# Kernel optimization log

Measured on AMD Instinct MI355X. Metric: run time of the kernel, lower is better.

## Reference

```python
import jax, jax.numpy as jnp
import numpy as np

EPS = 1e-9


def setup_inputs() -> dict:
    key = jax.random.key(0)
    k1, k2, k3, k4 = jax.random.split(key, 4)
    B, D, U = 1024, 512, 512
    x = jax.random.normal(k1, (B, D), dtype=jnp.float32)
    w = jax.random.normal(k2, (D, U), dtype=jnp.float32)
    p = jax.random.normal(k3, (D, U), dtype=jnp.float32)
    b = jax.random.normal(k4, (U,), dtype=jnp.float32)
    return {"x": x, "w": w, "p": p, "b": b}


def reference(x, w, p, b):
    # x: [B, D]; w, p: [D, U]; b: [U]
    xe = x[..., None] + EPS                      # [B, D, 1]
    abs_pow = jnp.abs(xe) ** p                   # [B, D, U]
    is_neg = xe < 0                              # [B, D, 1]
    odd_mask = jnp.mod(p, 2) != 0                # [D, U]
    signed = jnp.where(odd_mask & is_neg, -abs_pow, abs_pow)
    z = jnp.sum(w * signed, axis=1) + b          # [B, U]
    return z  # linear activation
```

## Files before the change

kernel.cpp:

```cpp
#include <hip/hip_runtime.h>
#include <math.h>

#define EPS 1e-9f

constexpr int Bn = 1024, Dn = 512, Un = 512;
constexpr int BM = 32;
constexpr int BU = 64;
constexpr int DK = 16;
constexpr int SPLITD = 8;
constexpr int DPB = Dn / SPLITD;
constexpr int NCHUNK = DPB / DK;

typedef float v4f __attribute__((ext_vector_type(4)));

__device__ __forceinline__ int swz(int d) { return ((d >> 2) & 3) << 3; }

template <bool USE_WS>
__global__ __launch_bounds__(256, 4) void power_layer(
    const float* __restrict__ x, const float* __restrict__ w,
    const float* __restrict__ p, const float* __restrict__ bias,
    float* __restrict__ outp)
{
    __shared__ float sL[DK][BM];
    __shared__ float sP[DK][BU];
    __shared__ float sW[DK][BU];
    __shared__ float sWX[DK][BU];

    const int tid = threadIdx.x;
    const int tx  = tid & 15;
    const int ty  = tid >> 4;
    const int tx4 = tx * 4;
    const int ty2 = ty * 2;
    const int ub = blockIdx.x * BU;
    const int bb = blockIdx.y * BM;
    const int d0 = blockIdx.z * DPB;

    const int xr  = tid >> 2;
    const int xdq = (tid & 3) << 2;
    const int pd  = tid >> 4;
    const int puq = (tid & 15) << 2;

    float4 xv = {}, pv = {}, wv = {};
    if (tid < 128)
        xv = *reinterpret_cast<const float4*>(&x[(size_t)(bb + xr) * Dn + d0 + xdq]);
    {
        const size_t gi = (size_t)(d0 + pd) * Un + ub + puq;
        pv = *reinterpret_cast<const float4*>(&p[gi]);
        wv = *reinterpret_cast<const float4*>(&w[gi]);
    }

    v4f acc[2] = {};

    for (int ch = 0; ch < NCHUNK; ++ch) {
        float Lenc[4];
        if (tid < 128) {
            const float* xs = reinterpret_cast<const float*>(&xv);
            #pragma unroll
            for (int j = 0; j < 4; ++j) {
                const float xe = xs[j] + EPS;
                const float La = __builtin_amdgcn_logf(fabsf(xe)) + 64.0f;
                Lenc[j] = (xe < 0.0f) ? -La : La;
            }
        }
        float4 wxv;
        {
            const float* ps  = reinterpret_cast<const float*>(&pv);
            const float* wsv = reinterpret_cast<const float*>(&wv);
            float* wxs = reinterpret_cast<float*>(&wxv);
            #pragma unroll
            for (int j = 0; j < 4; ++j) {
                const bool odd = (fmodf(ps[j], 2.0f) != 0.0f);
                wxs[j] = odd ? -wsv[j] : wsv[j];
            }
        }

        __syncthreads();
        if (tid < 128) {
            #pragma unroll
            for (int j = 0; j < 4; ++j) {
                const int dd = xdq + j;
                sL[dd][xr ^ swz(dd)] = Lenc[j];
            }
        }
        *reinterpret_cast<float4*>(&sP[pd][puq])  = pv;
        *reinterpret_cast<float4*>(&sW[pd][puq])  = wv;
        *reinterpret_cast<float4*>(&sWX[pd][puq]) = wxv;
        __syncthreads();

        if (ch + 1 < NCHUNK) {
            const int db = d0 + (ch + 1) * DK;
            if (tid < 128)
                xv = *reinterpret_cast<const float4*>(&x[(size_t)(bb + xr) * Dn + db + xdq]);
            const size_t gi = (size_t)(db + pd) * Un + ub + puq;
            pv = *reinterpret_cast<const float4*>(&p[gi]);
            wv = *reinterpret_cast<const float4*>(&w[gi]);
        }

        #pragma unroll 4
        for (int d = 0; d < DK; ++d) {
            const float2 Lv = *reinterpret_cast<const float2*>(&sL[d][ty2 ^ swz(d)]);
            const v4f    Pv = *reinterpret_cast<const v4f*>(&sP[d][tx4]);
            const float* Ls = reinterpret_cast<const float*>(&Lv);

            #pragma unroll
            for (int r = 0; r < 2; ++r) {
                const float Ld = fabsf(Ls[r]) - 64.0f;
                const bool  ng = Ls[r] < 0.0f;
                const v4f Wsel = *reinterpret_cast<const v4f*>(
                    ng ? &sWX[d][tx4] : &sW[d][tx4]);

                const v4f t = Pv * Ld;
                v4f e;
                #pragma unroll
                for (int c = 0; c < 4; ++c)
                    e[c] = __builtin_amdgcn_exp2f(t[c]);
                acc[r] = __builtin_elementwise_fma(Wsel, e, acc[r]);
            }
        }
        __syncthreads();
    }

    if (USE_WS) {
        float* dst = outp + ((size_t)blockIdx.z * Bn + bb + ty2) * Un + ub + tx4;
        #pragma unroll
        for (int r = 0; r < 2; ++r)
            *reinterpret_cast<v4f*>(dst + (size_t)r * Un) = acc[r];
    } else {
        if (blockIdx.z == 0) {
            const v4f bv = *reinterpret_cast<const v4f*>(&bias[ub + tx4]);
            #pragma unroll
            for (int r = 0; r < 2; ++r)
                acc[r] += bv;
        }
        #pragma unroll
        for (int r = 0; r < 2; ++r) {
            const int row = bb + ty2 + r;
            #pragma unroll
            for (int c = 0; c < 4; ++c)
                atomicAdd(&outp[(size_t)row * Un + ub + tx4 + c], acc[r][c]);
        }
    }
}

__global__ __launch_bounds__(256) void reduce_ws(
    const float* __restrict__ ws, const float* __restrict__ bias,
    float* __restrict__ out)
{
    const int nf4 = (Bn * Un) / 4;
    const int i = blockIdx.x * 256 + threadIdx.x;
    if (i >= nf4) return;
    const v4f* w4 = reinterpret_cast<const v4f*>(ws);
    v4f a = w4[i];
    #pragma unroll
    for (int z = 1; z < SPLITD; ++z)
        a += w4[(size_t)z * nf4 + i];
    a += reinterpret_cast<const v4f*>(bias)[i & (Un / 4 - 1)];
    reinterpret_cast<v4f*>(out)[i] = a;
}

extern "C" void kernel_launch(void* const* d_in, const int* in_sizes, int n_in,
                              void* d_out, int out_size, void* d_ws, size_t ws_size,
                              hipStream_t stream) {
    const float* x = (const float*)d_in[0];
    const float* w = (const float*)d_in[1];
    const float* p = (const float*)d_in[2];
    const float* b = (const float*)d_in[3];
    float* out = (float*)d_out;

    const dim3 grid(Un / BU, Bn / BM, SPLITD);
    const size_t need = (size_t)SPLITD * Bn * Un * sizeof(float);

    if (ws_size >= need) {
        float* wsf = (float*)d_ws;
        power_layer<true><<<grid, dim3(256), 0, stream>>>(x, w, p, b, wsf);
        reduce_ws<<<dim3((Bn * Un / 4 + 255) / 256), dim3(256), 0, stream>>>(wsf, b, out);
    } else {
        hipMemsetAsync(out, 0, (size_t)out_size * sizeof(float), stream);
        power_layer<false><<<grid, dim3(256), 0, stream>>>(x, w, p, b, out);
    }
}
```

Measured before the change: 109.5 us.

## Double-buffer P/W tiles and precompute full log(x) slab once per block

Precomputes the log-encoded x values for the block's whole D slice into shared memory up front, using all 256 threads, so x is no longer reloaded and re-logged per chunk. The P, W and sign-flipped W tiles are double-buffered, which cuts the per-chunk barriers from three to one. Shared memory grows, which may reduce occupancy, and the swizzle changes to suit the larger L array.

```diff
diff --git a/kernel.cpp b/kernel.cpp
--- a/kernel.cpp
+++ b/kernel.cpp
@@ -13,7 +13,7 @@
 
 typedef float v4f __attribute__((ext_vector_type(4)));
 
-__device__ __forceinline__ int swz(int d) { return ((d >> 2) & 3) << 3; }
+__device__ __forceinline__ int swzL(int d) { return ((d >> 3) & 7) << 2; }
 
 template <bool USE_WS>
 __global__ __launch_bounds__(256, 4) void power_layer(
@@ -21,10 +21,10 @@
     const float* __restrict__ p, const float* __restrict__ bias,
     float* __restrict__ outp)
 {
-    __shared__ float sL[DK][BM];
-    __shared__ float sP[DK][BU];
-    __shared__ float sW[DK][BU];
-    __shared__ float sWX[DK][BU];
+    __shared__ float sL[DPB][BM];
+    __shared__ float sP [2][DK][BU];
+    __shared__ float sW [2][DK][BU];
+    __shared__ float sWX[2][DK][BU];
 
     const int tid = threadIdx.x;
     const int tx  = tid & 15;
@@ -35,71 +35,67 @@
     const int bb = blockIdx.y * BM;
     const int d0 = blockIdx.z * DPB;
 
-    const int xr  = tid >> 2;
-    const int xdq = (tid & 3) << 2;
     const int pd  = tid >> 4;
     const int puq = (tid & 15) << 2;
 
-    float4 xv = {}, pv = {}, wv = {};
-    if (tid < 128)
-        xv = *reinterpret_cast<const float4*>(&x[(size_t)(bb + xr) * Dn + d0 + xdq]);
+    {
+        const int xr = tid >> 3;
+        const int xd = (tid & 7) << 3;
+        const int sw = (tid & 7) << 2;
+        const float* xrow = &x[(size_t)(bb + xr) * Dn + d0 + xd];
+        const float4 xa = *reinterpret_cast<const float4*>(xrow);
+        const float4 xb = *reinterpret_cast<const float4*>(xrow + 4);
+        const float* s0 = reinterpret_cast<const float*>(&xa);
+        const float* s1 = reinterpret_cast<const float*>(&xb);
+        #pragma unroll
+        for (int j = 0; j < 4; ++j) {
+            const float xe = s0[j] + EPS;
+            const float La = __builtin_amdgcn_logf(fabsf(xe)) + 64.0f;
+            sL[xd + j][xr ^ sw] = (xe < 0.0f) ? -La : La;
+        }
+        #pragma unroll
+        for (int j = 0; j < 4; ++j) {
+            const float xe = s1[j] + EPS;
+            const float La = __builtin_amdgcn_logf(fabsf(xe)) + 64.0f;
+            sL[xd + 4 + j][xr ^ sw] = (xe < 0.0f) ? -La : La;
+        }
+    }
     {
         const size_t gi = (size_t)(d0 + pd) * Un + ub + puq;
-        pv = *reinterpret_cast<const float4*>(&p[gi]);
-        wv = *reinterpret_cast<const float4*>(&w[gi]);
+        const float4 pv = *reinterpret_cast<const float4*>(&p[gi]);
+        const float4 wv = *reinterpret_cast<const float4*>(&w[gi]);
+        const float* ps  = reinterpret_cast<const float*>(&pv);
+        const float* wsv = reinterpret_cast<const float*>(&wv);
+        float4 wxv;
+        float* wxs = reinterpret_cast<float*>(&wxv);
+        #pragma unroll
+        for (int j = 0; j < 4; ++j) {
+            const bool odd = (fmodf(ps[j], 2.0f) != 0.0f);
+            wxs[j] = odd ? -wsv[j] : wsv[j];
+        }
+        *reinterpret_cast<float4*>(&sP [0][pd][puq]) = pv;
+        *reinterpret_cast<float4*>(&sW [0][pd][puq]) = wv;
+        *reinterpret_cast<float4*>(&sWX[0][pd][puq]) = wxv;
     }
+    __syncthreads();
 
     v4f acc[2] = {};
 
     for (int ch = 0; ch < NCHUNK; ++ch) {
-        float Lenc[4];
-        if (tid < 128) {
-            const float* xs = reinterpret_cast<const float*>(&xv);
-            #pragma unroll
-            for (int j = 0; j < 4; ++j) {
-                const float xe = xs[j] + EPS;
-                const float La = __builtin_amdgcn_logf(fabsf(xe)) + 64.0f;
-                Lenc[j] = (xe < 0.0f) ? -La : La;
-            }
-        }
-        float4 wxv;
-        {
-            const float* ps  = reinterpret_cast<const float*>(&pv);
-            const float* wsv = reinterpret_cast<const float*>(&wv);
-            float* wxs = reinterpret_cast<float*>(&wxv);
-            #pragma unroll
-            for (int j = 0; j < 4; ++j) {
-                const bool odd = (fmodf(ps[j], 2.0f) != 0.0f);
-                wxs[j] = odd ? -wsv[j] : wsv[j];
-            }
-        }
+        const int cur = ch & 1;
 
-        __syncthreads();
-        if (tid < 128) {
-            #pragma unroll
-            for (int j = 0; j < 4; ++j) {
-                const int dd = xdq + j;
-                sL[dd][xr ^ swz(dd)] = Lenc[j];
-            }
-        }
-        *reinterpret_cast<float4*>(&sP[pd][puq])  = pv;
-        *reinterpret_cast<float4*>(&sW[pd][puq])  = wv;
-        *reinterpret_cast<float4*>(&sWX[pd][puq]) = wxv;
-        __syncthreads();
-
+        float4 pv, wv;
         if (ch + 1 < NCHUNK) {
-            const int db = d0 + (ch + 1) * DK;
-            if (tid < 128)
-                xv = *reinterpret_cast<const float4*>(&x[(size_t)(bb + xr) * Dn + db + xdq]);
-            const size_t gi = (size_t)(db + pd) * Un + ub + puq;
+            const size_t gi = (size_t)(d0 + (ch + 1) * DK + pd) * Un + ub + puq;
             pv = *reinterpret_cast<const float4*>(&p[gi]);
             wv = *reinterpret_cast<const float4*>(&w[gi]);
         }
 
         #pragma unroll 4
         for (int d = 0; d < DK; ++d) {
-            const float2 Lv = *reinterpret_cast<const float2*>(&sL[d][ty2 ^ swz(d)]);
-            const v4f    Pv = *reinterpret_cast<const v4f*>(&sP[d][tx4]);
+            const int dd = ch * DK + d;
+            const float2 Lv = *reinterpret_cast<const float2*>(&sL[dd][ty2 ^ swzL(dd)]);
+            const v4f    Pv = *reinterpret_cast<const v4f*>(&sP[cur][d][tx4]);
             const float* Ls = reinterpret_cast<const float*>(&Lv);
 
             #pragma unroll
@@ -107,7 +103,7 @@
                 const float Ld = fabsf(Ls[r]) - 64.0f;
                 const bool  ng = Ls[r] < 0.0f;
                 const v4f Wsel = *reinterpret_cast<const v4f*>(
-                    ng ? &sWX[d][tx4] : &sW[d][tx4]);
+                    ng ? &sWX[cur][d][tx4] : &sW[cur][d][tx4]);
 
                 const v4f t = Pv * Ld;
                 v4f e;
@@ -117,7 +113,22 @@
                 acc[r] = __builtin_elementwise_fma(Wsel, e, acc[r]);
             }
         }
-        __syncthreads();
+
+        if (ch + 1 < NCHUNK) {
+            const float* ps  = reinterpret_cast<const float*>(&pv);
+            const float* wsv = reinterpret_cast<const float*>(&wv);
+            float4 wxv;
+            float* wxs = reinterpret_cast<float*>(&wxv);
+            #pragma unroll
+            for (int j = 0; j < 4; ++j) {
+                const bool odd = (fmodf(ps[j], 2.0f) != 0.0f);
+                wxs[j] = odd ? -wsv[j] : wsv[j];
+            }
+            *reinterpret_cast<float4*>(&sP [cur ^ 1][pd][puq]) = pv;
+            *reinterpret_cast<float4*>(&sW [cur ^ 1][pd][puq]) = wv;
+            *reinterpret_cast<float4*>(&sWX[cur ^ 1][pd][puq]) = wxv;
+            __syncthreads();
+        }
     }
 
     if (USE_WS) {
```

Result: no change. 108.1 us (-1.2%).
